# Kernel optimization log

Hardware: AMD Instinct MI355X
Metric: run time of the kernel (lower is better)

The kernel has to match this reference:

```python
import jax, jax.numpy as jnp
import numpy as np

D_MODEL = 1024
N_HEADS = 16
D_K = D_MODEL // N_HEADS


def setup_inputs() -> dict:
    key = jax.random.key(0)
    ks = jax.random.split(key, 5)
    x = jax.random.normal(ks[0], (4, 2048, D_MODEL), dtype=jnp.float32)
    # nn.Linear stores weight as [out, in]; we store transposed [in, out] for x @ W
    w_qkv = jax.random.normal(ks[1], (D_MODEL, 3 * D_MODEL), dtype=jnp.float32) / np.sqrt(D_MODEL)
    b_qkv = jnp.zeros((3 * D_MODEL,), dtype=jnp.float32)
    w_fc = jax.random.normal(ks[2], (D_MODEL, D_MODEL), dtype=jnp.float32) / np.sqrt(D_MODEL)
    b_fc = jnp.zeros((D_MODEL,), dtype=jnp.float32)
    ln_g = jnp.ones((D_MODEL,), dtype=jnp.float32)
    ln_b = jnp.zeros((D_MODEL,), dtype=jnp.float32)
    return {"x": x, "w_qkv": w_qkv, "b_qkv": b_qkv, "w_fc": w_fc, "b_fc": b_fc,
            "ln_g": ln_g, "ln_b": ln_b}


def _layernorm(x, g, b, eps=1e-5):
    mu = jnp.mean(x, axis=-1, keepdims=True)
    var = jnp.mean(jnp.square(x - mu), axis=-1, keepdims=True)
    return (x - mu) * jax.lax.rsqrt(var + eps) * g + b


def reference(x, w_qkv, b_qkv, w_fc, b_fc, ln_g, ln_b):
    residual = x
    xn = _layernorm(x, ln_g, ln_b)
    B, L, D = xn.shape
    qkv = xn @ w_qkv + b_qkv  # [B, L, 3D]
    q, k, v = jnp.split(qkv, 3, axis=-1)
    # b l (h d) -> b h l d
    def to_heads(t):
        return t.reshape(B, L, N_HEADS, D_K).transpose(0, 2, 1, 3)
    q, k, v = to_heads(q), to_heads(k), to_heads(v)
    scale = 1.0 / np.sqrt(D_K)
    scores = jnp.einsum('bhld,bhmd->bhlm', q, k) * scale  # [B,H,L,L]
    attn = jax.nn.softmax(scores, axis=-1)
    # dropout is identity in eval mode
    out = jnp.einsum('bhlm,bhmd->bhld', attn, v)  # [B,H,L,d]
    out = out.transpose(0, 2, 1, 3).reshape(B, L, D)  # b h l d -> b l (h d)
    out = out @ w_fc + b_fc
    return out + residual
```

## Files before the change

### kernel.cpp

```cpp
#include <hip/hip_runtime.h>
#include <hip/hip_bf16.h>
#include <cstdint>
#include <cstddef>

using bf16 = __hip_bfloat16;
typedef __attribute__((ext_vector_type(4))) float f32x4;
typedef __attribute__((ext_vector_type(8))) short bf16x8;

#define D_MODEL 1024
#define SEQ     2048
#define NB      4
#define NHEAD   16
#define DHEAD   64
#define NROWS   (NB * SEQ)

__device__ __forceinline__ void load_lds16(const void* g, void* l) {
  __builtin_amdgcn_global_load_lds(
      (const __attribute__((address_space(1))) unsigned int*)g,
      (__attribute__((address_space(3))) unsigned int*)l, 16, 0, 0);
}

__device__ __forceinline__ unsigned short f2bf(float f) {
  bf16 h = __float2bfloat16(f);
  return *(unsigned short*)&h;
}

__device__ __forceinline__ unsigned pk_trunc(float a, float b) {
  union { float f; unsigned u; } ca, cb;
  ca.f = a; cb.f = b;
  return (ca.u >> 16) | (cb.u & 0xffff0000u);
}

__global__ __launch_bounds__(256) void ln_kernel(
    const float* __restrict__ x, const float* __restrict__ g,
    const float* __restrict__ bb, bf16* __restrict__ xn) {
  int row  = blockIdx.x * 4 + (threadIdx.x >> 6);
  int lane = threadIdx.x & 63;
  const float4* xr = (const float4*)(x + (size_t)row * D_MODEL);
  float v[16], s = 0.f;
#pragma unroll
  for (int i = 0; i < 4; i++) {
    float4 t = xr[lane + 64 * i];
    v[4 * i] = t.x; v[4 * i + 1] = t.y; v[4 * i + 2] = t.z; v[4 * i + 3] = t.w;
    s += t.x + t.y + t.z + t.w;
  }
#pragma unroll
  for (int off = 32; off; off >>= 1) s += __shfl_xor(s, off, 64);
  float mean = s * (1.f / D_MODEL);
  float vs = 0.f;
#pragma unroll
  for (int i = 0; i < 16; i++) { float d = v[i] - mean; vs += d * d; }
#pragma unroll
  for (int off = 32; off; off >>= 1) vs += __shfl_xor(vs, off, 64);
  float rstd = rsqrtf(vs * (1.f / D_MODEL) + 1e-5f);
  ushort4* op = (ushort4*)(xn + (size_t)row * D_MODEL);
#pragma unroll
  for (int i = 0; i < 4; i++) {
    float4 gv = ((const float4*)g)[lane + 64 * i];
    float4 bv = ((const float4*)bb)[lane + 64 * i];
    ushort4 o;
    o.x = f2bf((v[4 * i]     - mean) * rstd * gv.x + bv.x);
    o.y = f2bf((v[4 * i + 1] - mean) * rstd * gv.y + bv.y);
    o.z = f2bf((v[4 * i + 2] - mean) * rstd * gv.z + bv.z);
    o.w = f2bf((v[4 * i + 3] - mean) * rstd * gv.w + bv.w);
    op[lane + 64 * i] = o;
  }
}

__global__ __launch_bounds__(256) void transpose_kernel(
    const float* __restrict__ w_qkv, bf16* __restrict__ wqkvT,
    const float* __restrict__ w_fc, bf16* __restrict__ wfcT) {
  __shared__ float tile[32][33];
  const float* in; bf16* out; int C, c0;
  if (blockIdx.x < 96) { in = w_qkv; out = wqkvT; C = 3072; c0 = blockIdx.x * 32; }
  else                 { in = w_fc;  out = wfcT;  C = 1024; c0 = (blockIdx.x - 96) * 32; }
  int r0 = blockIdx.y * 32;
  int tx = threadIdx.x & 31, ty = threadIdx.x >> 5;
  for (int i = ty; i < 32; i += 8)
    tile[i][tx] = in[(size_t)(r0 + i) * C + c0 + tx];
  __syncthreads();
  for (int i = ty; i < 32; i += 8)
    out[(size_t)(c0 + i) * 1024 + r0 + tx] = __float2bfloat16(tile[tx][i]);
}

__device__ __forceinline__ void store_ct(bf16* p, float v)  { *p = __float2bfloat16(v); }
__device__ __forceinline__ void store_ct(float* p, float v) { *p = v; }

template <int SPLIT, int RESID, typename CT>
__global__ __launch_bounds__(256) void gemm_bt(
    const bf16* __restrict__ A, const bf16* __restrict__ Bt,
    const float* __restrict__ bias, const float* __restrict__ resid,
    CT* __restrict__ C, bf16* __restrict__ vt, int M, int N, int K) {
  __shared__ __attribute__((aligned(16))) bf16 Alds[128 * 64];
  __shared__ __attribute__((aligned(16))) bf16 Blds[128 * 64];
  int tid = threadIdx.x, wave = tid >> 6, lane = tid & 63;
  int ntiles = N >> 7;
  int bm = blockIdx.x / ntiles, bn = blockIdx.x % ntiles;
  int m0 = bm << 7, n0 = bn << 7;
  int wm = (wave >> 1) << 6, wn = (wave & 1) << 6;
  int srow = tid >> 3;
  int sw8  = (((tid & 7) ^ (srow & 7)) << 3);
  int frow = lane & 15, quad = lane >> 4;
  const bf16* Ap[4];
  const bf16* Bp[4];
#pragma unroll
  for (int s = 0; s < 4; s++) {
    Ap[s] = A  + (size_t)(m0 + s * 32 + srow) * K + sw8;
    Bp[s] = Bt + (size_t)(n0 + s * 32 + srow) * K + sw8;
  }
  f32x4 acc[4][4] = {};
  for (int k0 = 0; k0 < K; k0 += 64) {
    __syncthreads();
#pragma unroll
    for (int s = 0; s < 4; s++) {
      load_lds16(Ap[s], (char*)Alds + s * 4096 + tid * 16);
      load_lds16(Bp[s], (char*)Blds + s * 4096 + tid * 16);
      Ap[s] += 64; Bp[s] += 64;
    }
    __syncthreads();
    bf16x8 af[4][2], bv[4][2];
#pragma unroll
    for (int i = 0; i < 4; i++)
#pragma unroll
      for (int kk = 0; kk < 2; kk++) {
        int e = (((kk * 4 + quad) ^ (frow & 7)) << 3);
        af[i][kk] = *(const bf16x8*)&Alds[(wm + i * 16 + frow) * 64 + e];
        bv[i][kk] = *(const bf16x8*)&Blds[(wn + i * 16 + frow) * 64 + e];
      }
#pragma unroll
    for (int i = 0; i < 4; i++)
#pragma unroll
      for (int j = 0; j < 4; j++) {
        acc[i][j] = __builtin_amdgcn_mfma_f32_16x16x32_bf16(af[i][0], bv[j][0], acc[i][j], 0, 0, 0);
        acc[i][j] = __builtin_amdgcn_mfma_f32_16x16x32_bf16(af[i][1], bv[j][1], acc[i][j], 0, 0, 0);
      }
  }
#pragma unroll
  for (int i = 0; i < 4; i++) {
    int row0 = m0 + wm + i * 16 + (quad << 2);
#pragma unroll
    for (int j = 0; j < 4; j++) {
      int col = n0 + wn + j * 16 + frow;
      float bvs = bias[col];
      if (SPLIT && col >= 2048) {
        int hd = col - 2048;
        int b = row0 >> 11, seq0 = row0 & 2047;
        int within = seq0 & 63, mt = within >> 4, q4 = (within >> 2) & 3;
        int pos = (seq0 & ~63) + ((mt >> 1) << 5) + (q4 << 3) + ((mt & 1) << 2);
        ushort4 pk;
        pk.x = f2bf(acc[i][j][0] + bvs);
        pk.y = f2bf(acc[i][j][1] + bvs);
        pk.z = f2bf(acc[i][j][2] + bvs);
        pk.w = f2bf(acc[i][j][3] + bvs);
        *(ushort4*)&vt[((size_t)(b * 1024 + hd)) * SEQ + pos] = pk;
      } else {
        int stride = SPLIT ? 2048 : N;
        float scale = (SPLIT && col < 1024) ? 0.18033688f : 1.0f;
#pragma unroll
        for (int r = 0; r < 4; r++) {
          size_t idx = (size_t)(row0 + r) * stride + col;
          float val = (acc[i][j][r] + bvs) * scale;
          if (RESID) val += resid[idx];
          store_ct(&C[idx], val);
        }
      }
    }
  }
}


__device__ __forceinline__ void stage_kv(
    const bf16* Kp0, const bf16* Kp1, const bf16* Vp0, const bf16* Vp1,
    bf16* KB, bf16* VB, int tid) {
  load_lds16(Kp0, (char*)KB + tid * 16);
  load_lds16(Kp1, (char*)KB + 4096 + tid * 16);
  load_lds16(Vp0, (char*)VB + tid * 16);
  load_lds16(Vp1, (char*)VB + 4096 + tid * 16);
}

__device__ __forceinline__ void kv_tile(
    const bf16* KL, const bf16* VL, int frow, int e0,
    const bf16x8 (&qf)[2][2], f32x4 (&l4)[2], f32x4 (&o)[4][2]) {
  f32x4 s[4][2] = {};
#pragma unroll
  for (int mt = 0; mt < 4; mt++) {
    bf16x8 af0 = *(const bf16x8*)&KL[(mt * 16 + frow) * 64 + e0];
    bf16x8 af1 = *(const bf16x8*)&KL[(mt * 16 + frow) * 64 + (e0 ^ 32)];
#pragma unroll
    for (int qt2 = 0; qt2 < 2; qt2++) {
      s[mt][qt2] = __builtin_amdgcn_mfma_f32_16x16x32_bf16(af0, qf[qt2][0], s[mt][qt2], 0, 0, 0);
      s[mt][qt2] = __builtin_amdgcn_mfma_f32_16x16x32_bf16(af1, qf[qt2][1], s[mt][qt2], 0, 0, 0);
    }
  }
  uint2 pk[2][4];
#pragma unroll
  for (int qt2 = 0; qt2 < 2; qt2++)
#pragma unroll
    for (int mt = 0; mt < 4; mt++) {
      f32x4 pv;
      pv[0] = __builtin_amdgcn_exp2f(s[mt][qt2][0]);
      pv[1] = __builtin_amdgcn_exp2f(s[mt][qt2][1]);
      pv[2] = __builtin_amdgcn_exp2f(s[mt][qt2][2]);
      pv[3] = __builtin_amdgcn_exp2f(s[mt][qt2][3]);
      l4[qt2] += pv;
      pk[qt2][mt].x = pk_trunc(pv[0], pv[1]);
      pk[qt2][mt].y = pk_trunc(pv[2], pv[3]);
    }
#pragma unroll
  for (int dt = 0; dt < 4; dt++) {
    bf16x8 vf0 = *(const bf16x8*)&VL[(dt * 16 + frow) * 64 + e0];
    bf16x8 vf1 = *(const bf16x8*)&VL[(dt * 16 + frow) * 64 + (e0 ^ 32)];
#pragma unroll
    for (int qt2 = 0; qt2 < 2; qt2++) {
      union { unsigned u[4]; bf16x8 v; } pf0, pf1;
      pf0.u[0] = pk[qt2][0].x; pf0.u[1] = pk[qt2][0].y;
      pf0.u[2] = pk[qt2][1].x; pf0.u[3] = pk[qt2][1].y;
      pf1.u[0] = pk[qt2][2].x; pf1.u[1] = pk[qt2][2].y;
      pf1.u[2] = pk[qt2][3].x; pf1.u[3] = pk[qt2][3].y;
      o[dt][qt2] = __builtin_amdgcn_mfma_f32_16x16x32_bf16(vf0, pf0.v, o[dt][qt2], 0, 0, 0);
      o[dt][qt2] = __builtin_amdgcn_mfma_f32_16x16x32_bf16(vf1, pf1.v, o[dt][qt2], 0, 0, 0);
    }
  }
}

__global__ __launch_bounds__(256, 4) void attn_kernel(
    const bf16* __restrict__ qk, const bf16* __restrict__ vt,
    bf16* __restrict__ aout) {
  int bh = blockIdx.x;
  int qt = blockIdx.y;
  int bb = bh >> 4, h = bh & 15;
  const bf16* Qg = qk + (size_t)bb * SEQ * 2048 + h * DHEAD;
  const bf16* Kg = Qg + D_MODEL;
  const bf16* Vg = vt + (size_t)bh * DHEAD * SEQ;

  __shared__ __attribute__((aligned(16))) bf16 Qlds[128 * 64];
  __shared__ __attribute__((aligned(16))) bf16 Klds[64 * 64];
  __shared__ __attribute__((aligned(16))) bf16 Vlds[64 * 64];

  int tid = threadIdx.x, wave = tid >> 6, lane = tid & 63;
  int prow = tid >> 3, pch = tid & 7;
  int lch8 = ((pch ^ (prow & 7)) << 3);
  int frow = lane & 15, quad = lane >> 4;
  int e0 = ((quad ^ (frow & 7)) << 3);
  int q0 = qt * 128;

  bf16* K0 = Klds;  bf16* V0 = Vlds;
  bf16* K1 = Qlds;  bf16* V1 = Qlds + 64 * 64;

  const bf16* Kp0 = Kg + (size_t)prow * 2048 + lch8;
  const bf16* Kp1 = Kg + (size_t)(32 + prow) * 2048 + lch8;
  const bf16* Vp0 = Vg + (size_t)prow * SEQ + lch8;
  const bf16* Vp1 = Vg + (size_t)(32 + prow) * SEQ + lch8;
  const size_t KT = (size_t)1 << 17;

#pragma unroll
  for (int s2 = 0; s2 < 4; s2++)
    load_lds16(Qg + (size_t)(q0 + s2 * 32 + prow) * 2048 + lch8,
               (char*)Qlds + s2 * 4096 + tid * 16);
  __syncthreads();
  bf16x8 qf[2][2];
#pragma unroll
  for (int qt2 = 0; qt2 < 2; qt2++)
#pragma unroll
    for (int kk = 0; kk < 2; kk++)
      qf[qt2][kk] =
          *(const bf16x8*)&Qlds[(wave * 32 + qt2 * 16 + frow) * 64 + (e0 ^ (kk * 32))];
  stage_kv(Kp0, Kp1, Vp0, Vp1, K0, V0, tid);
  __syncthreads();

  f32x4 l4[2] = {};
  f32x4 o[4][2] = {};

#pragma unroll 1
  for (int kt = 0; kt < 30; kt += 2) {
    stage_kv(Kp0 + KT, Kp1 + KT, Vp0 + 64, Vp1 + 64, K1, V1, tid);
    kv_tile(K0, V0, frow, e0, qf, l4, o);
    __syncthreads();
    stage_kv(Kp0 + 2 * KT, Kp1 + 2 * KT, Vp0 + 128, Vp1 + 128, K0, V0, tid);
    kv_tile(K1, V1, frow, e0, qf, l4, o);
    __syncthreads();
    Kp0 += 2 * KT; Kp1 += 2 * KT; Vp0 += 128; Vp1 += 128;
  }
  stage_kv(Kp0 + KT, Kp1 + KT, Vp0 + 64, Vp1 + 64, K1, V1, tid);
  kv_tile(K0, V0, frow, e0, qf, l4, o);
  __syncthreads();
  kv_tile(K1, V1, frow, e0, qf, l4, o);

  float linv[2];
#pragma unroll
  for (int qt2 = 0; qt2 < 2; qt2++) {
    float v = (l4[qt2][0] + l4[qt2][1]) + (l4[qt2][2] + l4[qt2][3]);
    v += __shfl_xor(v, 16, 64);
    v += __shfl_xor(v, 32, 64);
    linv[qt2] = 1.f / v;
  }

  __syncthreads();
  bf16* Tw = (wave == 0) ? Qlds
           : (wave == 1) ? Qlds + 32 * 80
           : (wave == 2) ? Klds : Vlds;
#pragma unroll
  for (int qt2 = 0; qt2 < 2; qt2++)
#pragma unroll
    for (int dt = 0; dt < 4; dt++) {
      ushort4 pk;
      pk.x = f2bf(o[dt][qt2][0] * linv[qt2]);
      pk.y = f2bf(o[dt][qt2][1] * linv[qt2]);
      pk.z = f2bf(o[dt][qt2][2] * linv[qt2]);
      pk.w = f2bf(o[dt][qt2][3] * linv[qt2]);
      *(ushort4*)&Tw[(qt2 * 16 + frow) * 80 + dt * 16 + quad * 4] = pk;
    }
  int rq = lane >> 1, d0 = (lane & 1) * 32;
  size_t grow = (size_t)(bb * SEQ + q0 + wave * 32 + rq);
#pragma unroll
  for (int i = 0; i < 4; i++) {
    bf16x8 v8 = *(const bf16x8*)&Tw[rq * 80 + d0 + i * 8];
    *(bf16x8*)&aout[grow * D_MODEL + h * DHEAD + d0 + i * 8] = v8;
  }
}

extern "C" void kernel_launch(void* const* d_in, const int* in_sizes, int n_in,
                              void* d_out, int out_size, void* d_ws, size_t ws_size,
                              hipStream_t stream) {
  const float* x     = (const float*)d_in[0];
  const float* w_qkv = (const float*)d_in[1];
  const float* b_qkv = (const float*)d_in[2];
  const float* w_fc  = (const float*)d_in[3];
  const float* b_fc  = (const float*)d_in[4];
  const float* ln_g  = (const float*)d_in[5];
  const float* ln_b  = (const float*)d_in[6];
  float* out = (float*)d_out;

  char* ws = (char*)d_ws;
  bf16* xn    = (bf16*)(ws);
  bf16* wqkvT = (bf16*)(ws + (16u << 20));
  bf16* wfcT  = (bf16*)(ws + (22u << 20));
  bf16* qk    = (bf16*)(ws + (24u << 20));
  bf16* vt    = (bf16*)(ws + (56u << 20));
  bf16* aout  = (bf16*)(ws);

  ln_kernel<<<NROWS / 4, 256, 0, stream>>>(x, ln_g, ln_b, xn);
  transpose_kernel<<<dim3(128, 32), 256, 0, stream>>>(w_qkv, wqkvT, w_fc, wfcT);
  gemm_bt<1, 0, bf16><<<(NROWS / 128) * (3 * D_MODEL / 128), 256, 0, stream>>>(
      xn, wqkvT, b_qkv, nullptr, qk, vt, NROWS, 3 * D_MODEL, D_MODEL);
  attn_kernel<<<dim3(NB * NHEAD, SEQ / 128), 256, 0, stream>>>(qk, vt, aout);
  gemm_bt<0, 1, float><<<(NROWS / 128) * (D_MODEL / 128), 256, 0, stream>>>(
      aout, wfcT, b_fc, x, out, nullptr, NROWS, D_MODEL, D_MODEL);
}
```

Measured before the change: 265.8 us.

## Software-pipeline attention loop: overlap QK of next tile with exp/PV of previous

```diff
diff --git a/kernel.cpp b/kernel.cpp
--- a/kernel.cpp
+++ b/kernel.cpp
@@ -178,49 +178,97 @@
   load_lds16(Vp1, (char*)VB + 4096 + tid * 16);
 }
 
-__device__ __forceinline__ void kv_tile(
-    const bf16* KL, const bf16* VL, int frow, int e0,
-    const bf16x8 (&qf)[2][2], f32x4 (&l4)[2], f32x4 (&o)[4][2]) {
-  f32x4 s[4][2] = {};
+__device__ __forceinline__ void qk_phase(
+    const bf16* KL, int frow, int e0, const bf16x8 (&qf)[2][2], f32x4 (&s)[4][2]) {
 #pragma unroll
   for (int mt = 0; mt < 4; mt++) {
     bf16x8 af0 = *(const bf16x8*)&KL[(mt * 16 + frow) * 64 + e0];
     bf16x8 af1 = *(const bf16x8*)&KL[(mt * 16 + frow) * 64 + (e0 ^ 32)];
 #pragma unroll
-    for (int qt2 = 0; qt2 < 2; qt2++) {
-      s[mt][qt2] = __builtin_amdgcn_mfma_f32_16x16x32_bf16(af0, qf[qt2][0], s[mt][qt2], 0, 0, 0);
-      s[mt][qt2] = __builtin_amdgcn_mfma_f32_16x16x32_bf16(af1, qf[qt2][1], s[mt][qt2], 0, 0, 0);
-    }
-  }
-  uint2 pk[2][4];
-#pragma unroll
-  for (int qt2 = 0; qt2 < 2; qt2++)
-#pragma unroll
-    for (int mt = 0; mt < 4; mt++) {
+    for (int q2 = 0; q2 < 2; q2++) {
+      s[mt][q2] = __builtin_amdgcn_mfma_f32_16x16x32_bf16(af0, qf[q2][0], s[mt][q2], 0, 0, 0);
+      s[mt][q2] = __builtin_amdgcn_mfma_f32_16x16x32_bf16(af1, qf[q2][1], s[mt][q2], 0, 0, 0);
+    }
+  }
+}
+
+__device__ __forceinline__ void exp_pv_phase(
+    const bf16* VL, int frow, int e0, const f32x4 (&s)[4][2],
+    const uint2 (&pki)[2][4], uint2 (&pko)[2][4], f32x4 (&l4)[2], f32x4 (&o)[4][2]) {
+#pragma unroll
+  for (int c = 0; c < 4; c++) {
+#pragma unroll
+    for (int q2 = 0; q2 < 2; q2++) {
       f32x4 pv;
-      pv[0] = __builtin_amdgcn_exp2f(s[mt][qt2][0]);
-      pv[1] = __builtin_amdgcn_exp2f(s[mt][qt2][1]);
-      pv[2] = __builtin_amdgcn_exp2f(s[mt][qt2][2]);
-      pv[3] = __builtin_amdgcn_exp2f(s[mt][qt2][3]);
-      l4[qt2] += pv;
-      pk[qt2][mt].x = pk_trunc(pv[0], pv[1]);
-      pk[qt2][mt].y = pk_trunc(pv[2], pv[3]);
-    }
-#pragma unroll
-  for (int dt = 0; dt < 4; dt++) {
-    bf16x8 vf0 = *(const bf16x8*)&VL[(dt * 16 + frow) * 64 + e0];
-    bf16x8 vf1 = *(const bf16x8*)&VL[(dt * 16 + frow) * 64 + (e0 ^ 32)];
-#pragma unroll
-    for (int qt2 = 0; qt2 < 2; qt2++) {
+      pv[0] = __builtin_amdgcn_exp2f(s[c][q2][0]);
+      pv[1] = __builtin_amdgcn_exp2f(s[c][q2][1]);
+      pv[2] = __builtin_amdgcn_exp2f(s[c][q2][2]);
+      pv[3] = __builtin_amdgcn_exp2f(s[c][q2][3]);
+      l4[q2] += pv;
+      pko[q2][c].x = pk_trunc(pv[0], pv[1]);
+      pko[q2][c].y = pk_trunc(pv[2], pv[3]);
+    }
+    bf16x8 vf0 = *(const bf16x8*)&VL[(c * 16 + frow) * 64 + e0];
+    bf16x8 vf1 = *(const bf16x8*)&VL[(c * 16 + frow) * 64 + (e0 ^ 32)];
+#pragma unroll
+    for (int q2 = 0; q2 < 2; q2++) {
       union { unsigned u[4]; bf16x8 v; } pf0, pf1;
-      pf0.u[0] = pk[qt2][0].x; pf0.u[1] = pk[qt2][0].y;
-      pf0.u[2] = pk[qt2][1].x; pf0.u[3] = pk[qt2][1].y;
-      pf1.u[0] = pk[qt2][2].x; pf1.u[1] = pk[qt2][2].y;
-      pf1.u[2] = pk[qt2][3].x; pf1.u[3] = pk[qt2][3].y;
-      o[dt][qt2] = __builtin_amdgcn_mfma_f32_16x16x32_bf16(vf0, pf0.v, o[dt][qt2], 0, 0, 0);
-      o[dt][qt2] = __builtin_amdgcn_mfma_f32_16x16x32_bf16(vf1, pf1.v, o[dt][qt2], 0, 0, 0);
-    }
-  }
+      pf0.u[0] = pki[q2][0].x; pf0.u[1] = pki[q2][0].y;
+      pf0.u[2] = pki[q2][1].x; pf0.u[3] = pki[q2][1].y;
+      pf1.u[0] = pki[q2][2].x; pf1.u[1] = pki[q2][2].y;
+      pf1.u[2] = pki[q2][3].x; pf1.u[3] = pki[q2][3].y;
+      o[c][q2] = __builtin_amdgcn_mfma_f32_16x16x32_bf16(vf0, pf0.v, o[c][q2], 0, 0, 0);
+      o[c][q2] = __builtin_amdgcn_mfma_f32_16x16x32_bf16(vf1, pf1.v, o[c][q2], 0, 0, 0);
+    }
+  }
+}
+
+__device__ __forceinline__ void exp_only(
+    const f32x4 (&s)[4][2], uint2 (&pko)[2][4], f32x4 (&l4)[2]) {
+#pragma unroll
+  for (int c = 0; c < 4; c++)
+#pragma unroll
+    for (int q2 = 0; q2 < 2; q2++) {
+      f32x4 pv;
+      pv[0] = __builtin_amdgcn_exp2f(s[c][q2][0]);
+      pv[1] = __builtin_amdgcn_exp2f(s[c][q2][1]);
+      pv[2] = __builtin_amdgcn_exp2f(s[c][q2][2]);
+      pv[3] = __builtin_amdgcn_exp2f(s[c][q2][3]);
+      l4[q2] += pv;
+      pko[q2][c].x = pk_trunc(pv[0], pv[1]);
+      pko[q2][c].y = pk_trunc(pv[2], pv[3]);
+    }
+}
+
+__device__ __forceinline__ void pv_only(
+    const bf16* VL, int frow, int e0, const uint2 (&pki)[2][4], f32x4 (&o)[4][2]) {
+#pragma unroll
+  for (int c = 0; c < 4; c++) {
+    bf16x8 vf0 = *(const bf16x8*)&VL[(c * 16 + frow) * 64 + e0];
+    bf16x8 vf1 = *(const bf16x8*)&VL[(c * 16 + frow) * 64 + (e0 ^ 32)];
+#pragma unroll
+    for (int q2 = 0; q2 < 2; q2++) {
+      union { unsigned u[4]; bf16x8 v; } pf0, pf1;
+      pf0.u[0] = pki[q2][0].x; pf0.u[1] = pki[q2][0].y;
+      pf0.u[2] = pki[q2][1].x; pf0.u[3] = pki[q2][1].y;
+      pf1.u[0] = pki[q2][2].x; pf1.u[1] = pki[q2][2].y;
+      pf1.u[2] = pki[q2][3].x; pf1.u[3] = pki[q2][3].y;
+      o[c][q2] = __builtin_amdgcn_mfma_f32_16x16x32_bf16(vf0, pf0.v, o[c][q2], 0, 0, 0);
+      o[c][q2] = __builtin_amdgcn_mfma_f32_16x16x32_bf16(vf1, pf1.v, o[c][q2], 0, 0, 0);
+    }
+  }
+}
+
+__device__ __forceinline__ void tile_body(
+    const bf16* Ks0, const bf16* Ks1, const bf16* Vs0, const bf16* Vs1,
+    bf16* Ksd, bf16* Vsd, const bf16* Krd, const bf16* Vrd,
+    int tid, int frow, int e0, const bf16x8 (&qf)[2][2],
+    const uint2 (&pki)[2][4], uint2 (&pko)[2][4], f32x4 (&l4)[2], f32x4 (&o)[4][2]) {
+  stage_kv(Ks0, Ks1, Vs0, Vs1, Ksd, Vsd, tid);
+  f32x4 s[4][2] = {};
+  qk_phase(Krd, frow, e0, qf, s);
+  exp_pv_phase(Vrd, frow, e0, s, pki, pko, l4, o);
+  __syncthreads();
 }
 
 __global__ __launch_bounds__(256, 4) void attn_kernel(
@@ -233,9 +281,12 @@
   const bf16* Kg = Qg + D_MODEL;
   const bf16* Vg = vt + (size_t)bh * DHEAD * SEQ;
 
-  __shared__ __attribute__((aligned(16))) bf16 Qlds[128 * 64];
-  __shared__ __attribute__((aligned(16))) bf16 Klds[64 * 64];
-  __shared__ __attribute__((aligned(16))) bf16 Vlds[64 * 64];
+  __shared__ __attribute__((aligned(16))) bf16 pool[20480];
+  bf16* Kb0 = pool;
+  bf16* Kb1 = pool + 4096;
+  bf16* V0  = pool + 8192;
+  bf16* V1  = pool + 12288;
+  bf16* V2  = pool + 16384;
 
   int tid = threadIdx.x, wave = tid >> 6, lane = tid & 63;
   int prow = tid >> 3, pch = tid & 7;
@@ -244,9 +295,6 @@
   int e0 = ((quad ^ (frow & 7)) << 3);
   int q0 = qt * 128;
 
-  bf16* K0 = Klds;  bf16* V0 = Vlds;
-  bf16* K1 = Qlds;  bf16* V1 = Qlds + 64 * 64;
-
   const bf16* Kp0 = Kg + (size_t)prow * 2048 + lch8;
   const bf16* Kp1 = Kg + (size_t)(32 + prow) * 2048 + lch8;
   const bf16* Vp0 = Vg + (size_t)prow * SEQ + lch8;
@@ -256,59 +304,79 @@
 #pragma unroll
   for (int s2 = 0; s2 < 4; s2++)
     load_lds16(Qg + (size_t)(q0 + s2 * 32 + prow) * 2048 + lch8,
-               (char*)Qlds + s2 * 4096 + tid * 16);
+               (char*)pool + s2 * 4096 + tid * 16);
   __syncthreads();
   bf16x8 qf[2][2];
 #pragma unroll
-  for (int qt2 = 0; qt2 < 2; qt2++)
+  for (int q2 = 0; q2 < 2; q2++)
 #pragma unroll
     for (int kk = 0; kk < 2; kk++)
-      qf[qt2][kk] =
-          *(const bf16x8*)&Qlds[(wave * 32 + qt2 * 16 + frow) * 64 + (e0 ^ (kk * 32))];
-  stage_kv(Kp0, Kp1, Vp0, Vp1, K0, V0, tid);
+      qf[q2][kk] =
+          *(const bf16x8*)&pool[(wave * 32 + q2 * 16 + frow) * 64 + (e0 ^ (kk * 32))];
+  __syncthreads();
+
+  stage_kv(Kp0, Kp1, Vp0, Vp1, Kb0, V0, tid);
+  stage_kv(Kp0 + KT, Kp1 + KT, Vp0 + 64, Vp1 + 64, Kb1, V1, tid);
   __syncthreads();
 
   f32x4 l4[2] = {};
   f32x4 o[4][2] = {};
+  uint2 pkA[2][4], pkB[2][4];
+
+  {
+    f32x4 s[4][2] = {};
+    qk_phase(Kb0, frow, e0, qf, s);
+    exp_only(s, pkB, l4);
+  }
+  __syncthreads();
+
+  Kp0 += KT; Kp1 += KT; Vp0 += 64; Vp1 += 64;
 
 #pragma unroll 1
-  for (int kt = 0; kt < 30; kt += 2) {
-    stage_kv(Kp0 + KT, Kp1 + KT, Vp0 + 64, Vp1 + 64, K1, V1, tid);
-    kv_tile(K0, V0, frow, e0, qf, l4, o);
-    __syncthreads();
-    stage_kv(Kp0 + 2 * KT, Kp1 + 2 * KT, Vp0 + 128, Vp1 + 128, K0, V0, tid);
-    kv_tile(K1, V1, frow, e0, qf, l4, o);
-    __syncthreads();
-    Kp0 += 2 * KT; Kp1 += 2 * KT; Vp0 += 128; Vp1 += 128;
-  }
-  stage_kv(Kp0 + KT, Kp1 + KT, Vp0 + 64, Vp1 + 64, K1, V1, tid);
-  kv_tile(K0, V0, frow, e0, qf, l4, o);
-  __syncthreads();
-  kv_tile(K1, V1, frow, e0, qf, l4, o);
+  for (int kt = 1; kt <= 25; kt += 6) {
+    tile_body(Kp0 + 1*KT, Kp1 + 1*KT, Vp0 + 1*64, Vp1 + 1*64, Kb0, V2, Kb1, V0,
+              tid, frow, e0, qf, pkB, pkA, l4, o);
+    tile_body(Kp0 + 2*KT, Kp1 + 2*KT, Vp0 + 2*64, Vp1 + 2*64, Kb1, V0, Kb0, V1,
+              tid, frow, e0, qf, pkA, pkB, l4, o);
+    tile_body(Kp0 + 3*KT, Kp1 + 3*KT, Vp0 + 3*64, Vp1 + 3*64, Kb0, V1, Kb1, V2,
+              tid, frow, e0, qf, pkB, pkA, l4, o);
+    tile_body(Kp0 + 4*KT, Kp1 + 4*KT, Vp0 + 4*64, Vp1 + 4*64, Kb1, V2, Kb0, V0,
+              tid, frow, e0, qf, pkA, pkB, l4, o);
+    tile_body(Kp0 + 5*KT, Kp1 + 5*KT, Vp0 + 5*64, Vp1 + 5*64, Kb0, V0, Kb1, V1,
+              tid, frow, e0, qf, pkB, pkA, l4, o);
+    tile_body(Kp0 + 6*KT, Kp1 + 6*KT, Vp0 + 6*64, Vp1 + 6*64, Kb1, V1, Kb0, V2,
+              tid, frow, e0, qf, pkA, pkB, l4, o);
+    Kp0 += 6 * KT; Kp1 += 6 * KT; Vp0 += 6 * 64; Vp1 += 6 * 64;
+  }
+
+  {
+    f32x4 s[4][2] = {};
+    qk_phase(Kb1, frow, e0, qf, s);
+    exp_pv_phase(V0, frow, e0, s, pkB, pkA, l4, o);
+  }
+  pv_only(V1, frow, e0, pkA, o);
 
   float linv[2];
 #pragma unroll
-  for (int qt2 = 0; qt2 < 2; qt2++) {
-    float v = (l4[qt2][0] + l4[qt2][1]) + (l4[qt2][2] + l4[qt2][3]);
+  for (int q2 = 0; q2 < 2; q2++) {
+    float v = (l4[q2][0] + l4[q2][1]) + (l4[q2][2] + l4[q2][3]);
     v += __shfl_xor(v, 16, 64);
     v += __shfl_xor(v, 32, 64);
-    linv[qt2] = 1.f / v;
-  }
-
-  __syncthreads();
-  bf16* Tw = (wave == 0) ? Qlds
-           : (wave == 1) ? Qlds + 32 * 80
-           : (wave == 2) ? Klds : Vlds;
-#pragma unroll
-  for (int qt2 = 0; qt2 < 2; qt2++)
+    linv[q2] = 1.f / v;
+  }
+
+  __syncthreads();
+  bf16* Tw = pool + wave * 2560;
+#pragma unroll
+  for (int q2 = 0; q2 < 2; q2++)
 #pragma unroll
     for (int dt = 0; dt < 4; dt++) {
       ushort4 pk;
-      pk.x = f2bf(o[dt][qt2][0] * linv[qt2]);
-      pk.y = f2bf(o[dt][qt2][1] * linv[qt2]);
-      pk.z = f2bf(o[dt][qt2][2] * linv[qt2]);
-      pk.w = f2bf(o[dt][qt2][3] * linv[qt2]);
-      *(ushort4*)&Tw[(qt2 * 16 + frow) * 80 + dt * 16 + quad * 4] = pk;
+      pk.x = f2bf(o[dt][q2][0] * linv[q2]);
+      pk.y = f2bf(o[dt][q2][1] * linv[q2]);
+      pk.z = f2bf(o[dt][q2][2] * linv[q2]);
+      pk.w = f2bf(o[dt][q2][3] * linv[q2]);
+      *(ushort4*)&Tw[(q2 * 16 + frow) * 80 + dt * 16 + quad * 4] = pk;
     }
   int rq = lane >> 1, d0 = (lane & 1) * 32;
   size_t grow = (size_t)(bb * SEQ + q0 + wave * 32 + rq);
```

Result: slower. 278.6 us (+4.8%).

## Replace QKV GEMM with 256x192-tile, 512-thread double-buffered MFMA kernel

Applied to the files above, without the earlier changes.

```diff
diff --git a/kernel.cpp b/kernel.cpp
--- a/kernel.cpp
+++ b/kernel.cpp
@@ -169,6 +169,155 @@
 }
 
 
+template <bool STG>
+__device__ __forceinline__ void ktile_qkv(
+    const bf16* Aw, const bf16* Bw,
+    bf16* Ad, bf16* Bd,
+    const bf16* const* Ab, const bf16* const* Bb, size_t koff,
+    int tid, int frow, int e_lo, int e_hi, f32x4 (&acc)[8][3]) {
+  __builtin_amdgcn_sched_barrier(0);
+  bf16x8 bv[3][2];
+#pragma unroll
+  for (int j = 0; j < 3; j++) {
+    bv[j][0] = *(const bf16x8*)&Bw[(j * 16 + frow) * 64 + e_lo];
+    bv[j][1] = *(const bf16x8*)&Bw[(j * 16 + frow) * 64 + e_hi];
+  }
+  bf16x8 a00 = *(const bf16x8*)&Aw[(frow) * 64 + e_lo];
+  bf16x8 a01 = *(const bf16x8*)&Aw[(frow) * 64 + e_hi];
+  bf16x8 a10 = *(const bf16x8*)&Aw[(16 + frow) * 64 + e_lo];
+  bf16x8 a11 = *(const bf16x8*)&Aw[(16 + frow) * 64 + e_hi];
+  if (STG) {
+#pragma unroll
+    for (int u = 0; u < 4; u++)
+      load_lds16(Ab[u] + koff, (char*)Ad + u * 8192 + tid * 16);
+#pragma unroll
+    for (int u = 0; u < 3; u++)
+      load_lds16(Bb[u] + koff, (char*)Bd + u * 8192 + tid * 16);
+  }
+  __builtin_amdgcn_s_barrier();
+  asm volatile("s_waitcnt lgkmcnt(0)" ::: "memory");
+  __builtin_amdgcn_sched_barrier(0);
+  __builtin_amdgcn_s_setprio(1);
+#pragma unroll
+  for (int j = 0; j < 3; j++) {
+    acc[0][j] = __builtin_amdgcn_mfma_f32_16x16x32_bf16(a00, bv[j][0], acc[0][j], 0, 0, 0);
+    acc[0][j] = __builtin_amdgcn_mfma_f32_16x16x32_bf16(a01, bv[j][1], acc[0][j], 0, 0, 0);
+    acc[1][j] = __builtin_amdgcn_mfma_f32_16x16x32_bf16(a10, bv[j][0], acc[1][j], 0, 0, 0);
+    acc[1][j] = __builtin_amdgcn_mfma_f32_16x16x32_bf16(a11, bv[j][1], acc[1][j], 0, 0, 0);
+  }
+  __builtin_amdgcn_s_setprio(0);
+  __builtin_amdgcn_s_barrier();
+#pragma unroll
+  for (int p = 1; p < 4; p++) {
+    bf16x8 c00 = *(const bf16x8*)&Aw[((2 * p) * 16 + frow) * 64 + e_lo];
+    bf16x8 c01 = *(const bf16x8*)&Aw[((2 * p) * 16 + frow) * 64 + e_hi];
+    bf16x8 c10 = *(const bf16x8*)&Aw[((2 * p + 1) * 16 + frow) * 64 + e_lo];
+    bf16x8 c11 = *(const bf16x8*)&Aw[((2 * p + 1) * 16 + frow) * 64 + e_hi];
+    __builtin_amdgcn_s_barrier();
+    asm volatile("s_waitcnt lgkmcnt(0)" ::: "memory");
+    __builtin_amdgcn_sched_barrier(0);
+    __builtin_amdgcn_s_setprio(1);
+#pragma unroll
+    for (int j = 0; j < 3; j++) {
+      acc[2 * p][j]     = __builtin_amdgcn_mfma_f32_16x16x32_bf16(c00, bv[j][0], acc[2 * p][j], 0, 0, 0);
+      acc[2 * p][j]     = __builtin_amdgcn_mfma_f32_16x16x32_bf16(c01, bv[j][1], acc[2 * p][j], 0, 0, 0);
+      acc[2 * p + 1][j] = __builtin_amdgcn_mfma_f32_16x16x32_bf16(c10, bv[j][0], acc[2 * p + 1][j], 0, 0, 0);
+      acc[2 * p + 1][j] = __builtin_amdgcn_mfma_f32_16x16x32_bf16(c11, bv[j][1], acc[2 * p + 1][j], 0, 0, 0);
+    }
+    __builtin_amdgcn_s_setprio(0);
+    if (p == 3) {
+      asm volatile("s_waitcnt vmcnt(0)" ::: "memory");
+      __builtin_amdgcn_sched_barrier(0);
+    }
+    __builtin_amdgcn_s_barrier();
+  }
+}
+
+__global__ __launch_bounds__(512, 2) void gemm256_qkv(
+    const bf16* __restrict__ A, const bf16* __restrict__ Bt,
+    const float* __restrict__ bias, bf16* __restrict__ C, bf16* __restrict__ vt) {
+  __shared__ __attribute__((aligned(16))) bf16 AL0[256 * 64];
+  __shared__ __attribute__((aligned(16))) bf16 AL1[256 * 64];
+  __shared__ __attribute__((aligned(16))) bf16 BL0[192 * 64];
+  __shared__ __attribute__((aligned(16))) bf16 BL1[192 * 64];
+
+  int bid = blockIdx.x;
+  int logical = (bid & 7) * 64 + (bid >> 3);
+  int bm = logical >> 4;
+  int bn = logical & 15;
+  int m0 = bm * 256, n0 = bn * 192;
+
+  int tid = threadIdx.x, wave = tid >> 6, lane = tid & 63;
+  int wm = (wave >> 2) * 128;
+  int wn = (wave & 3) * 48;
+  int srow = tid >> 3;
+  int sw8 = (((tid & 7) ^ (srow & 7)) << 3);
+  int frow = lane & 15, quad = lane >> 4;
+  int e_lo = ((quad ^ (frow & 7)) << 3);
+  int e_hi = (((4 + quad) ^ (frow & 7)) << 3);
+
+  const bf16* Ab[4];
+  const bf16* Bb[3];
+#pragma unroll
+  for (int u = 0; u < 4; u++) Ab[u] = A + (size_t)(m0 + u * 64 + srow) * 1024 + sw8;
+#pragma unroll
+  for (int u = 0; u < 3; u++) Bb[u] = Bt + (size_t)(n0 + u * 64 + srow) * 1024 + sw8;
+
+#pragma unroll
+  for (int u = 0; u < 4; u++) load_lds16(Ab[u], (char*)AL0 + u * 8192 + tid * 16);
+#pragma unroll
+  for (int u = 0; u < 3; u++) load_lds16(Bb[u], (char*)BL0 + u * 8192 + tid * 16);
+  asm volatile("s_waitcnt vmcnt(0)" ::: "memory");
+  __builtin_amdgcn_sched_barrier(0);
+  __builtin_amdgcn_s_barrier();
+
+  f32x4 acc[8][3] = {};
+  const bf16* A0w = AL0 + wm * 64;
+  const bf16* B0w = BL0 + wn * 64;
+  const bf16* A1w = AL1 + wm * 64;
+  const bf16* B1w = BL1 + wn * 64;
+
+  size_t ko = 64;
+#pragma unroll 1
+  for (int t2 = 0; t2 < 14; t2 += 2) {
+    ktile_qkv<true>(A0w, B0w, AL1, BL1, Ab, Bb, ko,      tid, frow, e_lo, e_hi, acc);
+    ktile_qkv<true>(A1w, B1w, AL0, BL0, Ab, Bb, ko + 64, tid, frow, e_lo, e_hi, acc);
+    ko += 128;
+  }
+  ktile_qkv<true >(A0w, B0w, AL1, BL1, Ab, Bb, ko, tid, frow, e_lo, e_hi, acc);
+  ktile_qkv<false>(A1w, B1w, AL0, BL0, Ab, Bb, 0,  tid, frow, e_lo, e_hi, acc);
+
+#pragma unroll
+  for (int i = 0; i < 8; i++) {
+    int row0 = m0 + wm + i * 16 + (quad << 2);
+#pragma unroll
+    for (int j = 0; j < 3; j++) {
+      int col = n0 + wn + j * 16 + frow;
+      float bvs = bias[col];
+      if (col >= 2048) {
+        int hd = col - 2048;
+        int b = row0 >> 11, seq0 = row0 & 2047;
+        int within = seq0 & 63, mt = within >> 4, q4 = (within >> 2) & 3;
+        int pos = (seq0 & ~63) + ((mt >> 1) << 5) + (q4 << 3) + ((mt & 1) << 2);
+        ushort4 pk;
+        pk.x = f2bf(acc[i][j][0] + bvs);
+        pk.y = f2bf(acc[i][j][1] + bvs);
+        pk.z = f2bf(acc[i][j][2] + bvs);
+        pk.w = f2bf(acc[i][j][3] + bvs);
+        *(ushort4*)&vt[((size_t)(b * 1024 + hd)) * SEQ + pos] = pk;
+      } else {
+        float scale = (col < 1024) ? 0.18033688f : 1.0f;
+#pragma unroll
+        for (int r = 0; r < 4; r++) {
+          size_t idx = (size_t)(row0 + r) * 2048 + col;
+          C[idx] = __float2bfloat16((acc[i][j][r] + bvs) * scale);
+        }
+      }
+    }
+  }
+}
+
+
 __device__ __forceinline__ void stage_kv(
     const bf16* Kp0, const bf16* Kp1, const bf16* Vp0, const bf16* Vp1,
     bf16* KB, bf16* VB, int tid) {
@@ -341,8 +490,7 @@
 
   ln_kernel<<<NROWS / 4, 256, 0, stream>>>(x, ln_g, ln_b, xn);
   transpose_kernel<<<dim3(128, 32), 256, 0, stream>>>(w_qkv, wqkvT, w_fc, wfcT);
-  gemm_bt<1, 0, bf16><<<(NROWS / 128) * (3 * D_MODEL / 128), 256, 0, stream>>>(
-      xn, wqkvT, b_qkv, nullptr, qk, vt, NROWS, 3 * D_MODEL, D_MODEL);
+  gemm256_qkv<<<512, 512, 0, stream>>>(xn, wqkvT, b_qkv, qk, vt);
   attn_kernel<<<dim3(NB * NHEAD, SEQ / 128), 256, 0, stream>>>(qk, vt, aout);
   gemm_bt<0, 1, float><<<(NROWS / 128) * (D_MODEL / 128), 256, 0, stream>>>(
       aout, wfcT, b_fc, x, out, nullptr, NROWS, D_MODEL, D_MODEL);
```

Result: no change. 270.7 us (+1.8%).

## Restructure GEMM into per-wave private LDS tiles with barrier-free prefetch

Applied to the files above, without the earlier changes.

```diff
diff --git a/kernel.cpp b/kernel.cpp
--- a/kernel.cpp
+++ b/kernel.cpp
@@ -86,47 +86,58 @@
 __device__ __forceinline__ void store_ct(bf16* p, float v)  { *p = __float2bfloat16(v); }
 __device__ __forceinline__ void store_ct(float* p, float v) { *p = v; }
 
-template <int SPLIT, int RESID, typename CT>
-__global__ __launch_bounds__(256) void gemm_bt(
+template <int K, int SPLIT, int RESID, typename CT>
+__global__ __launch_bounds__(256) void gemm_wa(
     const bf16* __restrict__ A, const bf16* __restrict__ Bt,
     const float* __restrict__ bias, const float* __restrict__ resid,
-    CT* __restrict__ C, bf16* __restrict__ vt, int M, int N, int K) {
-  __shared__ __attribute__((aligned(16))) bf16 Alds[128 * 64];
-  __shared__ __attribute__((aligned(16))) bf16 Blds[128 * 64];
+    CT* __restrict__ C, bf16* __restrict__ vt, int M, int N) {
+  __shared__ __attribute__((aligned(16))) bf16 lds[4 * 8192];
   int tid = threadIdx.x, wave = tid >> 6, lane = tid & 63;
   int ntiles = N >> 7;
   int bm = blockIdx.x / ntiles, bn = blockIdx.x % ntiles;
   int m0 = bm << 7, n0 = bn << 7;
   int wm = (wave >> 1) << 6, wn = (wave & 1) << 6;
-  int srow = tid >> 3;
-  int sw8  = (((tid & 7) ^ (srow & 7)) << 3);
+  int row8 = lane >> 3, ch8 = lane & 7;
+  int sw8 = ((ch8 ^ row8) << 3);
   int frow = lane & 15, quad = lane >> 4;
-  const bf16* Ap[4];
-  const bf16* Bp[4];
-#pragma unroll
-  for (int s = 0; s < 4; s++) {
-    Ap[s] = A  + (size_t)(m0 + s * 32 + srow) * K + sw8;
-    Bp[s] = Bt + (size_t)(n0 + s * 32 + srow) * K + sw8;
-  }
+  bf16* Aw = lds + wave * 8192;
+  bf16* Bw = Aw + 4096;
+
+  const bf16* Asrc = A  + (size_t)(m0 + wm + row8) * K + sw8;
+  const bf16* Bsrc = Bt + (size_t)(n0 + wn + row8) * K + sw8;
+
+  auto stage = [&](const bf16* As, const bf16* Bs) {
+#pragma unroll
+    for (int c = 0; c < 8; c++)
+      load_lds16(As + (size_t)(8 * c) * K, (char*)Aw + c * 1024 + lane * 16);
+#pragma unroll
+    for (int c = 0; c < 8; c++)
+      load_lds16(Bs + (size_t)(8 * c) * K, (char*)Bw + c * 1024 + lane * 16);
+  };
+
+  stage(Asrc, Bsrc);
+  Asrc += 64; Bsrc += 64;
+  asm volatile("s_waitcnt vmcnt(0)" ::: "memory");
+  __builtin_amdgcn_sched_barrier(0);
+
   f32x4 acc[4][4] = {};
-  for (int k0 = 0; k0 < K; k0 += 64) {
-    __syncthreads();
-#pragma unroll
-    for (int s = 0; s < 4; s++) {
-      load_lds16(Ap[s], (char*)Alds + s * 4096 + tid * 16);
-      load_lds16(Bp[s], (char*)Blds + s * 4096 + tid * 16);
-      Ap[s] += 64; Bp[s] += 64;
-    }
-    __syncthreads();
+#pragma unroll 1
+  for (int t = 0; t < K / 64 - 1; t++) {
     bf16x8 af[4][2], bv[4][2];
 #pragma unroll
     for (int i = 0; i < 4; i++)
 #pragma unroll
       for (int kk = 0; kk < 2; kk++) {
         int e = (((kk * 4 + quad) ^ (frow & 7)) << 3);
-        af[i][kk] = *(const bf16x8*)&Alds[(wm + i * 16 + frow) * 64 + e];
-        bv[i][kk] = *(const bf16x8*)&Blds[(wn + i * 16 + frow) * 64 + e];
-      }
+        af[i][kk] = *(const bf16x8*)&Aw[(i * 16 + frow) * 64 + e];
+        bv[i][kk] = *(const bf16x8*)&Bw[(i * 16 + frow) * 64 + e];
+      }
+    asm volatile("s_waitcnt lgkmcnt(0)" ::: "memory");
+    __builtin_amdgcn_sched_barrier(0);
+    stage(Asrc, Bsrc);
+    Asrc += 64; Bsrc += 64;
+    __builtin_amdgcn_sched_barrier(0);
+    __builtin_amdgcn_s_setprio(1);
 #pragma unroll
     for (int i = 0; i < 4; i++)
 #pragma unroll
@@ -134,7 +145,31 @@
         acc[i][j] = __builtin_amdgcn_mfma_f32_16x16x32_bf16(af[i][0], bv[j][0], acc[i][j], 0, 0, 0);
         acc[i][j] = __builtin_amdgcn_mfma_f32_16x16x32_bf16(af[i][1], bv[j][1], acc[i][j], 0, 0, 0);
       }
-  }
+    __builtin_amdgcn_s_setprio(0);
+    asm volatile("s_waitcnt vmcnt(0)" ::: "memory");
+    __builtin_amdgcn_sched_barrier(0);
+  }
+  {
+    bf16x8 af[4][2], bv[4][2];
+#pragma unroll
+    for (int i = 0; i < 4; i++)
+#pragma unroll
+      for (int kk = 0; kk < 2; kk++) {
+        int e = (((kk * 4 + quad) ^ (frow & 7)) << 3);
+        af[i][kk] = *(const bf16x8*)&Aw[(i * 16 + frow) * 64 + e];
+        bv[i][kk] = *(const bf16x8*)&Bw[(i * 16 + frow) * 64 + e];
+      }
+    asm volatile("s_waitcnt lgkmcnt(0)" ::: "memory");
+    __builtin_amdgcn_sched_barrier(0);
+#pragma unroll
+    for (int i = 0; i < 4; i++)
+#pragma unroll
+      for (int j = 0; j < 4; j++) {
+        acc[i][j] = __builtin_amdgcn_mfma_f32_16x16x32_bf16(af[i][0], bv[j][0], acc[i][j], 0, 0, 0);
+        acc[i][j] = __builtin_amdgcn_mfma_f32_16x16x32_bf16(af[i][1], bv[j][1], acc[i][j], 0, 0, 0);
+      }
+  }
+
 #pragma unroll
   for (int i = 0; i < 4; i++) {
     int row0 = m0 + wm + i * 16 + (quad << 2);
@@ -341,9 +376,9 @@
 
   ln_kernel<<<NROWS / 4, 256, 0, stream>>>(x, ln_g, ln_b, xn);
   transpose_kernel<<<dim3(128, 32), 256, 0, stream>>>(w_qkv, wqkvT, w_fc, wfcT);
-  gemm_bt<1, 0, bf16><<<(NROWS / 128) * (3 * D_MODEL / 128), 256, 0, stream>>>(
-      xn, wqkvT, b_qkv, nullptr, qk, vt, NROWS, 3 * D_MODEL, D_MODEL);
+  gemm_wa<1024, 1, 0, bf16><<<(NROWS / 128) * (3 * D_MODEL / 128), 256, 0, stream>>>(
+      xn, wqkvT, b_qkv, nullptr, qk, vt, NROWS, 3 * D_MODEL);
   attn_kernel<<<dim3(NB * NHEAD, SEQ / 128), 256, 0, stream>>>(qk, vt, aout);
-  gemm_bt<0, 1, float><<<(NROWS / 128) * (D_MODEL / 128), 256, 0, stream>>>(
-      aout, wfcT, b_fc, x, out, nullptr, NROWS, D_MODEL, D_MODEL);
-}
+  gemm_wa<1024, 0, 1, float><<<(NROWS / 128) * (D_MODEL / 128), 256, 0, stream>>>(
+      aout, wfcT, b_fc, x, out, nullptr, NROWS, D_MODEL);
+}
```

Result: slower. 282.8 us (+6.4%).
